# Performance work log

Hardware: AMD Instinct MI355X
Metric: run time of the kernel (lower is better)

Reference implementation:

```python
import jax, jax.numpy as jnp
import numpy as np

N_STEPS = 100
TAU_S = 5.0  # network_config['tau_s']
SHAPE = (16, 128, 16, 16, N_STEPS)  # [B, C, H, W, T]


def psp(target):
    """Leaky-integrator postsynaptic potential: syn_t = syn_{t-1}*(1-1/tau_s) + x_t, emit syn_t/tau_s."""
    x = jnp.moveaxis(target, -1, 0)  # time-major [T, B, C, H, W]
    decay = 1.0 - 1.0 / TAU_S

    def step(syn, xt):
        syn = syn * decay + xt
        return syn, syn / TAU_S

    _, syns = jax.lax.scan(step, jnp.zeros_like(x[0]), x)
    return jnp.moveaxis(syns, 0, -1)  # back to [B, C, H, W, T]


def setup_inputs() -> dict:
    key = jax.random.key(0)
    k1, k2 = jax.random.split(key)
    outputs = jax.random.normal(k1, SHAPE, dtype=jnp.float32) * 0.1
    target = (jax.random.uniform(k2, SHAPE) < 0.2).astype(jnp.float32)
    return {"outputs": outputs, "target": target}


def reference(outputs, target):
    # SpikeLoss.spike_kernel: 0.5 * sum((outputs - psp(target))**2)
    delta = outputs - psp(target)
    return 0.5 * jnp.sum(delta ** 2)
```

## Files before the change

### kernel.cpp

```cpp
#include <hip/hip_runtime.h>


#define T_STEPS 100
#define SEG 25
#define NPB 64
#define BLOCK 256
#define N_NEURONS (16 * 128 * 16 * 16)
#define GRID_P (N_NEURONS / NPB)
#define F4_PER_ARR (NPB * T_STEPS / 4)

#define GLOBAL_AS __attribute__((address_space(1)))
#define LDS_AS __attribute__((address_space(3)))

__device__ __forceinline__ void async_f4(const float4* g, float4* l) {
  __builtin_amdgcn_global_load_lds((const GLOBAL_AS void*)g, (LDS_AS void*)l,
                                   16, 0, 0);
}

__device__ __forceinline__ float block_loss(const float* __restrict__ outputs,
                                            const float* __restrict__ target) {
  __shared__ float xbuf[NPB * T_STEPS];
  __shared__ float obuf[NPB * T_STEPS];
  __shared__ float lE[NPB * 4];
  __shared__ float wsum[BLOCK / 64];

  const int tid = threadIdx.x;
  const size_t base = (size_t)blockIdx.x * (NPB * T_STEPS);
  const float4* gt = reinterpret_cast<const float4*>(target + base);
  const float4* go = reinterpret_cast<const float4*>(outputs + base);
  float4* lx4 = reinterpret_cast<float4*>(xbuf);
  float4* lo4 = reinterpret_cast<float4*>(obuf);

#pragma unroll
  for (int it = 0; it < 6; ++it) async_f4(gt + it * 256 + tid, lx4 + it * 256 + tid);
  if (tid < F4_PER_ARR - 1536) async_f4(gt + 1536 + tid, lx4 + 1536 + tid);
#pragma unroll
  for (int it = 0; it < 6; ++it) async_f4(go + it * 256 + tid, lo4 + it * 256 + tid);
  if (tid < F4_PER_ARR - 1536) async_f4(go + 1536 + tid, lo4 + 1536 + tid);

  __syncthreads();

  const int n = tid >> 2;
  const int s = tid & 3;
  const float* xrow = xbuf + n * T_STEPS + s * SEG;
  float E = 0.f;
#pragma unroll
  for (int j = 0; j < SEG; ++j) E = fmaf(E, 0.8f, xrow[j]);
  lE[tid] = E;

  __syncthreads();

  const float A25 = 3.77789319e-3f;
  const float A50 = 1.42724769e-5f;
  float carry = 0.f;
  if (s >= 1) carry = lE[tid - 1];
  if (s >= 2) carry = fmaf(A25, lE[tid - 2], carry);
  if (s >= 3) carry = fmaf(A50, lE[tid - 3], carry);

  const float* orow = obuf + n * T_STEPS + s * SEG;
  float syn = carry;
  float acc = 0.f;
#pragma unroll
  for (int j = 0; j < SEG; ++j) {
    syn = fmaf(syn, 0.8f, xrow[j]);
    float d = fmaf(-0.2f, syn, orow[j]);
    acc = fmaf(d, d, acc);
  }

#pragma unroll
  for (int off = 32; off > 0; off >>= 1) acc += __shfl_down(acc, off, 64);
  const int lane = tid & 63;
  const int wid = tid >> 6;
  if (lane == 0) wsum[wid] = acc;
  __syncthreads();
  return wsum[0] + wsum[1] + wsum[2] + wsum[3];
}

__global__ __launch_bounds__(BLOCK, 3) void spike_loss_partial(
    const float* __restrict__ outputs,
    const float* __restrict__ target,
    float* __restrict__ partial) {
  float blocksum = block_loss(outputs, target);
  if (threadIdx.x == 0) partial[blockIdx.x] = blocksum;
}

__global__ __launch_bounds__(256) void spike_loss_final(
    const float* __restrict__ partial, float* __restrict__ out, int nparts) {
  float acc = 0.0f;
  for (int i = threadIdx.x; i < nparts; i += 256) acc += partial[i];
#pragma unroll
  for (int off = 32; off > 0; off >>= 1) acc += __shfl_down(acc, off, 64);
  __shared__ float wsum[4];
  const int lane = threadIdx.x & 63;
  const int wid = threadIdx.x >> 6;
  if (lane == 0) wsum[wid] = acc;
  __syncthreads();
  if (threadIdx.x == 0) out[0] = 0.5f * (wsum[0] + wsum[1] + wsum[2] + wsum[3]);
}

__global__ __launch_bounds__(BLOCK, 3) void spike_loss_atomic(
    const float* __restrict__ outputs,
    const float* __restrict__ target,
    float* __restrict__ out) {
  float blocksum = block_loss(outputs, target);
  if (threadIdx.x == 0) atomicAdd(out, 0.5f * blocksum);
}

extern "C" void kernel_launch(void* const* d_in, const int* in_sizes, int n_in,
                              void* d_out, int out_size, void* d_ws, size_t ws_size,
                              hipStream_t stream) {
  const float* outputs = (const float*)d_in[0];
  const float* target = (const float*)d_in[1];
  float* out = (float*)d_out;

  if (ws_size >= GRID_P * sizeof(float)) {
    float* partial = (float*)d_ws;
    spike_loss_partial<<<GRID_P, BLOCK, 0, stream>>>(outputs, target, partial);
    spike_loss_final<<<1, 256, 0, stream>>>(partial, out, GRID_P);
  } else {
    hipMemsetAsync(out, 0, sizeof(float), stream);
    spike_loss_atomic<<<GRID_P, BLOCK, 0, stream>>>(outputs, target, out);
  }
}
```

Measured before the change: 409.2 us.

## Shrink blocks to one wavefront and exchange segment carries via shuffles

Each block now handles 16 neurons with a single 64-thread wavefront instead of 64 neurons across four wavefronts. The segment-carry exchange moves from LDS plus a barrier to __shfl_up, and the cross-wave LDS reduction disappears, so the barriers after the scan and at the end are gone. Target values are also kept in registers between the two passes instead of being read from LDS twice. In exchange the grid is four times larger, so the final reduction kernel has four times as many partials to sum, and block-scheduling overhead rises.

```diff
diff --git a/kernel.cpp b/kernel.cpp
--- a/kernel.cpp
+++ b/kernel.cpp
@@ -3,11 +3,12 @@
 
 #define T_STEPS 100
 #define SEG 25
-#define NPB 64
-#define BLOCK 256
+#define NPB 16
+#define BLOCK 64
 #define N_NEURONS (16 * 128 * 16 * 16)
 #define GRID_P (N_NEURONS / NPB)
-#define F4_PER_ARR (NPB * T_STEPS / 4)
+#define FLOATS_PB (NPB * T_STEPS)
+#define F4_PB (FLOATS_PB / 4)
 
 #define GLOBAL_AS __attribute__((address_space(1)))
 #define LDS_AS __attribute__((address_space(3)))
@@ -17,71 +18,66 @@
                                    16, 0, 0);
 }
 
-__device__ __forceinline__ float block_loss(const float* __restrict__ outputs,
-                                            const float* __restrict__ target) {
-  __shared__ float xbuf[NPB * T_STEPS];
-  __shared__ float obuf[NPB * T_STEPS];
-  __shared__ float lE[NPB * 4];
-  __shared__ float wsum[BLOCK / 64];
+__device__ __forceinline__ float tile_loss(const float* __restrict__ outputs,
+                                           const float* __restrict__ target) {
+  __shared__ float xbuf[FLOATS_PB];
+  __shared__ float obuf[FLOATS_PB];
 
   const int tid = threadIdx.x;
-  const size_t base = (size_t)blockIdx.x * (NPB * T_STEPS);
+  const size_t base = (size_t)blockIdx.x * FLOATS_PB;
   const float4* gt = reinterpret_cast<const float4*>(target + base);
   const float4* go = reinterpret_cast<const float4*>(outputs + base);
   float4* lx4 = reinterpret_cast<float4*>(xbuf);
   float4* lo4 = reinterpret_cast<float4*>(obuf);
 
 #pragma unroll
-  for (int it = 0; it < 6; ++it) async_f4(gt + it * 256 + tid, lx4 + it * 256 + tid);
-  if (tid < F4_PER_ARR - 1536) async_f4(gt + 1536 + tid, lx4 + 1536 + tid);
+  for (int it = 0; it < 6; ++it) async_f4(gt + it * 64 + tid, lx4 + it * 64 + tid);
+  if (tid < F4_PB - 384) async_f4(gt + 384 + tid, lx4 + 384 + tid);
 #pragma unroll
-  for (int it = 0; it < 6; ++it) async_f4(go + it * 256 + tid, lo4 + it * 256 + tid);
-  if (tid < F4_PER_ARR - 1536) async_f4(go + 1536 + tid, lo4 + 1536 + tid);
+  for (int it = 0; it < 6; ++it) async_f4(go + it * 64 + tid, lo4 + it * 64 + tid);
+  if (tid < F4_PB - 384) async_f4(go + 384 + tid, lo4 + 384 + tid);
 
   __syncthreads();
 
   const int n = tid >> 2;
   const int s = tid & 3;
   const float* xrow = xbuf + n * T_STEPS + s * SEG;
+  float x[SEG];
+#pragma unroll
+  for (int j = 0; j < SEG; ++j) x[j] = xrow[j];
   float E = 0.f;
 #pragma unroll
-  for (int j = 0; j < SEG; ++j) E = fmaf(E, 0.8f, xrow[j]);
-  lE[tid] = E;
+  for (int j = 0; j < SEG; ++j) E = fmaf(E, 0.8f, x[j]);
 
-  __syncthreads();
-
-  const float A25 = 3.77789319e-3f;
-  const float A50 = 1.42724769e-5f;
+  float c1 = __shfl_up(E, 1);
+  float c2 = __shfl_up(E, 2);
+  float c3 = __shfl_up(E, 3);
   float carry = 0.f;
-  if (s >= 1) carry = lE[tid - 1];
-  if (s >= 2) carry = fmaf(A25, lE[tid - 2], carry);
-  if (s >= 3) carry = fmaf(A50, lE[tid - 3], carry);
+  if (s >= 1) carry = c1;
+  if (s >= 2) carry = fmaf(3.77789319e-3f, c2, carry);
+  if (s >= 3) carry = fmaf(1.42724769e-5f, c3, carry);
 
   const float* orow = obuf + n * T_STEPS + s * SEG;
   float syn = carry;
   float acc = 0.f;
 #pragma unroll
   for (int j = 0; j < SEG; ++j) {
-    syn = fmaf(syn, 0.8f, xrow[j]);
+    syn = fmaf(syn, 0.8f, x[j]);
     float d = fmaf(-0.2f, syn, orow[j]);
     acc = fmaf(d, d, acc);
   }
 
 #pragma unroll
   for (int off = 32; off > 0; off >>= 1) acc += __shfl_down(acc, off, 64);
-  const int lane = tid & 63;
-  const int wid = tid >> 6;
-  if (lane == 0) wsum[wid] = acc;
-  __syncthreads();
-  return wsum[0] + wsum[1] + wsum[2] + wsum[3];
+  return acc;
 }
 
 __global__ __launch_bounds__(BLOCK, 3) void spike_loss_partial(
     const float* __restrict__ outputs,
     const float* __restrict__ target,
     float* __restrict__ partial) {
-  float blocksum = block_loss(outputs, target);
-  if (threadIdx.x == 0) partial[blockIdx.x] = blocksum;
+  float acc = tile_loss(outputs, target);
+  if (threadIdx.x == 0) partial[blockIdx.x] = acc;
 }
 
 __global__ __launch_bounds__(256) void spike_loss_final(
@@ -102,8 +98,8 @@
     const float* __restrict__ outputs,
     const float* __restrict__ target,
     float* __restrict__ out) {
-  float blocksum = block_loss(outputs, target);
-  if (threadIdx.x == 0) atomicAdd(out, 0.5f * blocksum);
+  float acc = tile_loss(outputs, target);
+  if (threadIdx.x == 0) atomicAdd(out, 0.5f * acc);
 }
 
 extern "C" void kernel_launch(void* const* d_in, const int* in_sizes, int n_in,
```

Measured after the change: 430.3 us. 5.1% more time.
